# Performance work log

Hardware: AMD Instinct MI355X
Metric: run time of the kernel (lower is better)

## Reference

```python
import jax, jax.numpy as jnp
import numpy as np

EPS = 1e-12  # matches F.normalize default eps

def _l2norm(x):
    n = jnp.linalg.norm(x, axis=-1, keepdims=True)
    return x / jnp.maximum(n, EPS)

def setup_inputs() -> dict:
    key = jax.random.key(0)
    kq, kk, kv = jax.random.split(key, 3)
    B, N, D = 16384, 8192, 1024
    return {
        "query": jax.random.normal(kq, (B, D), dtype=jnp.float32),
        "keys": jax.random.normal(kk, (N, D), dtype=jnp.float32),
        "values": jax.random.normal(kv, (N, D), dtype=jnp.float32),
        "k": 4,
    }

def reference(query, keys, values, k):
    # cosine similarity: (B, N)
    qn = _l2norm(query)
    kn = _l2norm(keys)
    sim = jnp.einsum('bd,nd->bn', qn, kn)
    actual_k = min(k, sim.shape[1])
    topk_sim, topk_idx = jax.lax.top_k(sim, actual_k)     # (B, k)
    weights = jax.nn.softmax(topk_sim, axis=-1)            # (B, k)
    topk_vals = values[topk_idx]                           # (B, k, D)
    return jnp.einsum('bk,bkd->bd', weights, topk_vals)    # (B, D)
```

## Files before the change

kernel.cpp:

```cpp
#include <hip/hip_runtime.h>
#include <hip/hip_bf16.h>
#include <math.h>


#define D_DIM 1024
#define SLICES 8
#define BQ 128
#define BK 128
#define BD 64
#define TLIST 4
#define CAND_PER_Q (SLICES * TLIST)

typedef float f32x4 __attribute__((ext_vector_type(4)));
typedef short s16x8 __attribute__((ext_vector_type(8)));

typedef const __attribute__((address_space(1))) void* as1cv;
typedef __attribute__((address_space(3))) void* as3v;

__device__ __forceinline__ void gload_lds16(const void* g, void* l) {
    __builtin_amdgcn_global_load_lds((as1cv)g, (as3v)l, 16, 0, 0);
}

__device__ __forceinline__ unsigned short f2bf(float x) {
    unsigned int u;
    __builtin_memcpy(&u, &x, 4);
    unsigned int r = (u + 0x7fffu + ((u >> 16) & 1u)) >> 16;
    return (unsigned short)r;
}

__global__ __launch_bounds__(256) void nrm_kernel(
    const float* __restrict__ q, const float* __restrict__ kmat,
    unsigned short* __restrict__ qn, unsigned short* __restrict__ kn,
    float* __restrict__ inv_qn, float* __restrict__ inv_kn, int B, int N) {
    int wid = threadIdx.x >> 6, lane = threadIdx.x & 63;
    int row = blockIdx.x * 4 + wid;
    if (row >= B + N) return;
    const float* src;
    unsigned short* dst;
    float* invp;
    if (row < B) {
        src = q + (size_t)row * D_DIM; dst = qn + (size_t)row * D_DIM; invp = inv_qn + row;
    } else {
        int r = row - B;
        src = kmat + (size_t)r * D_DIM; dst = kn + (size_t)r * D_DIM; invp = inv_kn + r;
    }
    float4 v[4];
    float ss = 0.f;
#pragma unroll
    for (int c = 0; c < 4; ++c) {
        v[c] = *(const float4*)(src + c * 256 + lane * 4);
        ss += v[c].x * v[c].x + v[c].y * v[c].y + v[c].z * v[c].z + v[c].w * v[c].w;
    }
#pragma unroll
    for (int m = 1; m < 64; m <<= 1) ss += __shfl_xor(ss, m, 64);
    float s = 1.0f / fmaxf(sqrtf(ss), 1e-12f);
    if (lane == 0) *invp = s;
#pragma unroll
    for (int c = 0; c < 4; ++c) {
        ushort4 o;
        o.x = f2bf(v[c].x * s); o.y = f2bf(v[c].y * s);
        o.z = f2bf(v[c].z * s); o.w = f2bf(v[c].w * s);
        *(ushort4*)(dst + c * 256 + lane * 4) = o;
    }
}

__global__ __launch_bounds__(256, 4) void score_kernel(
    const unsigned short* __restrict__ qn, const unsigned short* __restrict__ kn,
    float* __restrict__ cand_s, int* __restrict__ cand_i, int B, int N) {
    __shared__ __attribute__((aligned(16))) unsigned char smem[33792];
    unsigned short* Kt = (unsigned short*)smem;
    unsigned short* Qt = (unsigned short*)(smem + 16384);
    float* ms = (float*)smem;
    int* mi = (int*)(smem + 16896);

    int bx = blockIdx.x;
    int qblk = bx >> 3, slice = bx & 7;
    int tid = threadIdx.x, wid = tid >> 6, lane = tid & 63;
    int wr = wid & 1, wc = wid >> 1;
    int slice_len = N / SLICES;
    int kbase0 = slice * slice_len;
    int qbase = qblk * BQ;
    int lg = lane >> 4;

    float ts[4][TLIST];
    int   ti[4][TLIST];
#pragma unroll
    for (int cg = 0; cg < 4; ++cg)
#pragma unroll
        for (int t = 0; t < TLIST; ++t) { ts[cg][t] = -1e30f; ti[cg][t] = 0; }

    for (int kt = 0; kt < slice_len / BK; ++kt) {
        int kb = kbase0 + kt * BK;
        f32x4 acc[4][4];
#pragma unroll
        for (int a = 0; a < 4; ++a)
#pragma unroll
            for (int b = 0; b < 4; ++b) acc[a][b] = (f32x4){0.f, 0.f, 0.f, 0.f};

        for (int dc = 0; dc < D_DIM / BD; ++dc) {
            int db = dc * BD;
#pragma unroll
            for (int i = 0; i < 4; ++i) {
                int te = (i * 4 + wid) * 64 + lane;
                int r = te >> 3, sl = te & 7;
                int c = (sl ^ (r & 7)) * 8;
                gload_lds16(kn + (size_t)(kb + r) * D_DIM + db + c, &Kt[(i * 4 + wid) * 512]);
            }
#pragma unroll
            for (int i = 0; i < 4; ++i) {
                int te = (i * 4 + wid) * 64 + lane;
                int r = te >> 3, sl = te & 7;
                int c = (sl ^ (r & 7)) * 8;
                gload_lds16(qn + (size_t)(qbase + r) * D_DIM + db + c, &Qt[(i * 4 + wid) * 512]);
            }
            __syncthreads();
#pragma unroll
            for (int ks = 0; ks < 2; ++ks) {
                int kslot = ks * 4 + lg;
                s16x8 afr[4], bfr[4];
#pragma unroll
                for (int rb = 0; rb < 4; ++rb) {
                    int row = wr * 64 + rb * 16 + (lane & 15);
                    afr[rb] = *(const s16x8*)&Kt[row * BD + ((kslot ^ (row & 7)) * 8)];
                }
#pragma unroll
                for (int cg = 0; cg < 4; ++cg) {
                    int row = wc * 64 + cg * 16 + (lane & 15);
                    bfr[cg] = *(const s16x8*)&Qt[row * BD + ((kslot ^ (row & 7)) * 8)];
                }
#pragma unroll
                for (int rb = 0; rb < 4; ++rb)
#pragma unroll
                    for (int cg = 0; cg < 4; ++cg)
                        acc[rb][cg] = __builtin_amdgcn_mfma_f32_16x16x32_bf16(
                            afr[rb], bfr[cg], acc[rb][cg], 0, 0, 0);
            }
            __syncthreads();
        }
#pragma unroll
        for (int rb = 0; rb < 4; ++rb) {
#pragma unroll
            for (int j = 0; j < 4; ++j) {
                int key = kb + wr * 64 + rb * 16 + (lg << 2) + j;
#pragma unroll
                for (int cg = 0; cg < 4; ++cg) {
                    float s = acc[rb][cg][j];
                    if (s > ts[cg][TLIST - 1]) {
                        int id = key;
#pragma unroll
                        for (int t = 0; t < TLIST; ++t) {
                            bool c = s > ts[cg][t];
                            float hi = c ? s : ts[cg][t];
                            float lo = c ? ts[cg][t] : s;
                            int ih = c ? id : ti[cg][t];
                            int il = c ? ti[cg][t] : id;
                            ts[cg][t] = hi; ti[cg][t] = ih; s = lo; id = il;
                        }
                    }
                }
            }
        }
    }

    __syncthreads();
#pragma unroll
    for (int cg = 0; cg < 4; ++cg) {
        int ql = wc * 64 + cg * 16 + (lane & 15);
        int slot = wr * 16 + lg * 4;
#pragma unroll
        for (int t = 0; t < TLIST; ++t) {
            ms[ql * 33 + slot + t] = ts[cg][t];
            mi[ql * 33 + slot + t] = ti[cg][t];
        }
    }
    __syncthreads();
    if (tid < BQ) {
        float bs[4] = {-1e30f, -1e30f, -1e30f, -1e30f};
        int bi4[4] = {0, 0, 0, 0};
#pragma unroll
        for (int s = 0; s < 32; ++s) {
            float v = ms[tid * 33 + s];
            int id = mi[tid * 33 + s];
            if (v > bs[3]) {
#pragma unroll
                for (int t = 0; t < 4; ++t) {
                    bool c = v > bs[t];
                    float hi = c ? v : bs[t];
                    float lo = c ? bs[t] : v;
                    int ih = c ? id : bi4[t];
                    int il = c ? bi4[t] : id;
                    bs[t] = hi; bi4[t] = ih; v = lo; id = il;
                }
            }
        }
        size_t base = (size_t)(qbase + tid) * CAND_PER_Q + slice * TLIST;
#pragma unroll
        for (int t = 0; t < 4; ++t) {
            cand_s[base + t] = bs[t];
            cand_i[base + t] = bi4[t];
        }
    }
}

__global__ __launch_bounds__(256) void final_kernel(
    const float* __restrict__ q, const float* __restrict__ kmat, const float* __restrict__ vmat,
    const float* __restrict__ inv_qn, const float* __restrict__ inv_kn,
    const float* __restrict__ cand_s, const int* __restrict__ cand_i,
    const int* __restrict__ kptr, float* __restrict__ out, int B, int N) {
    int wid = threadIdx.x >> 6, lane = threadIdx.x & 63;
    int qi = blockIdx.x * 4 + wid;
    int kk = *kptr;
    kk = kk < 1 ? 1 : (kk > 8 ? 8 : kk);

    size_t cb = (size_t)qi * CAND_PER_Q;
    float cs = lane < 32 ? cand_s[cb + lane] : -1e30f;
    int ci = lane < 32 ? cand_i[cb + lane] : 0x7fffffff;

    int rank = 0;
#pragma unroll
    for (int j = 0; j < 32; ++j) {
        float sj = __shfl(cs, j, 64);
        int ij = __shfl(ci, j, 64);
        rank += ((sj > cs) || (sj == cs && ij < ci)) ? 1 : 0;
    }
    int sel[8];
#pragma unroll
    for (int r = 0; r < 8; ++r) {
        unsigned long long m = __ballot(lane < 32 && rank == r);
        int ln = (int)__builtin_ctzll(m);
        sel[r] = __shfl(ci, ln, 64);
    }

    const float* qrow = q + (size_t)qi * D_DIM;
    float4 qv[4];
#pragma unroll
    for (int c = 0; c < 4; ++c) qv[c] = *(const float4*)(qrow + c * 256 + lane * 4);
    const float* kr[8];
#pragma unroll
    for (int r = 0; r < 8; ++r) kr[r] = kmat + (size_t)sel[r] * D_DIM;
    float p[8];
#pragma unroll
    for (int r = 0; r < 8; ++r) p[r] = 0.f;
#pragma unroll
    for (int e = 0; e < 4; ++e) {
#pragma unroll
        for (int r = 0; r < 8; ++r) {
            float4 kv = *(const float4*)(kr[r] + e * 256 + lane * 4);
            p[r] += qv[e].x * kv.x + qv[e].y * kv.y + qv[e].z * kv.z + qv[e].w * kv.w;
        }
    }
#pragma unroll
    for (int m = 1; m < 64; m <<= 1) {
#pragma unroll
        for (int r = 0; r < 8; ++r) p[r] += __shfl_xor(p[r], m, 64);
    }
    float invq = inv_qn[qi];
    float exsc[8];
#pragma unroll
    for (int r = 0; r < 8; ++r) exsc[r] = p[r] * invq * inv_kn[sel[r]];

    float wl[8]; int il[8]; bool used[8];
#pragma unroll
    for (int i = 0; i < 8; ++i) used[i] = false;
#pragma unroll
    for (int i = 0; i < 8; ++i) {
        int bj = 0; float bv = -1e30f; int bidx = 0x7fffffff;
#pragma unroll
        for (int j = 0; j < 8; ++j) {
            if (!used[j] && (exsc[j] > bv || (exsc[j] == bv && sel[j] < bidx))) {
                bv = exsc[j]; bidx = sel[j]; bj = j;
            }
        }
        used[bj] = true; wl[i] = bv; il[i] = bidx;
    }
    float m0 = wl[0], ssum = 0.f;
#pragma unroll
    for (int i = 0; i < 8; ++i) {
        wl[i] = (i < kk) ? __expf(wl[i] - m0) : 0.f;
        ssum += wl[i];
    }
    float rs = 1.0f / ssum;

    float4 o[4];
#pragma unroll
    for (int c = 0; c < 4; ++c) o[c] = (float4){0.f, 0.f, 0.f, 0.f};
#pragma unroll
    for (int i = 0; i < 8; ++i) {
        if (i < kk) {
            const float* vrow = vmat + (size_t)il[i] * D_DIM;
            float wi = wl[i] * rs;
#pragma unroll
            for (int c = 0; c < 4; ++c) {
                float4 vv = *(const float4*)(vrow + c * 256 + lane * 4);
                o[c].x += wi * vv.x; o[c].y += wi * vv.y;
                o[c].z += wi * vv.z; o[c].w += wi * vv.w;
            }
        }
    }
    float* orow = out + (size_t)qi * D_DIM;
#pragma unroll
    for (int c = 0; c < 4; ++c) *(float4*)(orow + c * 256 + lane * 4) = o[c];
}

extern "C" void kernel_launch(void* const* d_in, const int* in_sizes, int n_in,
                              void* d_out, int out_size, void* d_ws, size_t ws_size,
                              hipStream_t stream) {
    const float* q = (const float*)d_in[0];
    const float* kmat = (const float*)d_in[1];
    const float* vmat = (const float*)d_in[2];
    const int* kptr = (const int*)d_in[3];
    float* out = (float*)d_out;
    int B = in_sizes[0] / D_DIM;
    int N = in_sizes[1] / D_DIM;

    char* ws = (char*)d_ws;
    size_t off = 0;
    unsigned short* qn = (unsigned short*)(ws + off); off += (size_t)B * D_DIM * 2;
    unsigned short* kn = (unsigned short*)(ws + off); off += (size_t)N * D_DIM * 2;
    float* inv_qn = (float*)(ws + off); off += (size_t)B * 4;
    float* inv_kn = (float*)(ws + off); off += (size_t)N * 4;
    float* cand_s = (float*)(ws + off); off += (size_t)B * CAND_PER_Q * 4;
    int* cand_i = (int*)(ws + off); off += (size_t)B * CAND_PER_Q * 4;

    int rows = B + N;
    nrm_kernel<<<dim3((rows + 3) / 4), dim3(256), 0, stream>>>(q, kmat, qn, kn, inv_qn, inv_kn, B, N);
    score_kernel<<<dim3((B / BQ) * SLICES), dim3(256), 0, stream>>>(qn, kn, cand_s, cand_i, B, N);
    final_kernel<<<dim3(B / 4), dim3(256), 0, stream>>>(q, kmat, vmat, inv_qn, inv_kn,
                                                        cand_s, cand_i, kptr, out, B, N);
}
```

Measured before the change: 683.0 us.

## Enlarge score tiles to 256x256 with double-buffered LDS and wave-level top-k skip

New measurement: 651.1 us. 4.7% less time.

```diff
diff --git a/kernel.cpp b/kernel.cpp
--- a/kernel.cpp
+++ b/kernel.cpp
@@ -5,8 +5,8 @@
 
 #define D_DIM 1024
 #define SLICES 8
-#define BQ 128
-#define BK 128
+#define BQ 256
+#define BK 256
 #define BD 64
 #define TLIST 4
 #define CAND_PER_Q (SLICES * TLIST)
@@ -64,23 +64,21 @@
     }
 }
 
-__global__ __launch_bounds__(256, 4) void score_kernel(
+__global__ __launch_bounds__(512, 2) void score_kernel(
     const unsigned short* __restrict__ qn, const unsigned short* __restrict__ kn,
     float* __restrict__ cand_s, int* __restrict__ cand_i, int B, int N) {
-    __shared__ __attribute__((aligned(16))) unsigned char smem[33792];
-    unsigned short* Kt = (unsigned short*)smem;
-    unsigned short* Qt = (unsigned short*)(smem + 16384);
+    __shared__ __attribute__((aligned(16))) unsigned char smem[131072];
     float* ms = (float*)smem;
-    int* mi = (int*)(smem + 16896);
+    int* mi = (int*)(smem + 33792);
 
     int bx = blockIdx.x;
     int qblk = bx >> 3, slice = bx & 7;
     int tid = threadIdx.x, wid = tid >> 6, lane = tid & 63;
     int wr = wid & 1, wc = wid >> 1;
+    int lg = lane >> 4, l15 = lane & 15;
     int slice_len = N / SLICES;
     int kbase0 = slice * slice_len;
     int qbase = qblk * BQ;
-    int lg = lane >> 4;
 
     float ts[4][TLIST];
     int   ti[4][TLIST];
@@ -89,72 +87,90 @@
 #pragma unroll
         for (int t = 0; t < TLIST; ++t) { ts[cg][t] = -1e30f; ti[cg][t] = 0; }
 
+    auto STAGE = [&](int c, int kb, int db) {
+        unsigned short* KtD = (unsigned short*)(smem + c * 65536);
+        unsigned short* QtD = (unsigned short*)(smem + 32768 + c * 65536);
+#pragma unroll
+        for (int i = 0; i < 4; ++i) {
+            int te = i * 512 + tid;
+            int r = te >> 3, sl = te & 7;
+            int col = (sl ^ (r & 7)) * 8;
+            gload_lds16(kn + (size_t)(kb + r) * D_DIM + db + col, &KtD[i * 4096 + wid * 512]);
+        }
+#pragma unroll
+        for (int i = 0; i < 4; ++i) {
+            int te = i * 512 + tid;
+            int r = te >> 3, sl = te & 7;
+            int col = (sl ^ (r & 7)) * 8;
+            gload_lds16(qn + (size_t)(qbase + r) * D_DIM + db + col, &QtD[i * 4096 + wid * 512]);
+        }
+    };
+
     for (int kt = 0; kt < slice_len / BK; ++kt) {
         int kb = kbase0 + kt * BK;
-        f32x4 acc[4][4];
-#pragma unroll
-        for (int a = 0; a < 4; ++a)
+        f32x4 acc[8][4];
+#pragma unroll
+        for (int a = 0; a < 8; ++a)
 #pragma unroll
             for (int b = 0; b < 4; ++b) acc[a][b] = (f32x4){0.f, 0.f, 0.f, 0.f};
 
+        STAGE(0, kb, 0);
+        __syncthreads();
+        int cur = 0;
         for (int dc = 0; dc < D_DIM / BD; ++dc) {
-            int db = dc * BD;
-#pragma unroll
-            for (int i = 0; i < 4; ++i) {
-                int te = (i * 4 + wid) * 64 + lane;
-                int r = te >> 3, sl = te & 7;
-                int c = (sl ^ (r & 7)) * 8;
-                gload_lds16(kn + (size_t)(kb + r) * D_DIM + db + c, &Kt[(i * 4 + wid) * 512]);
-            }
-#pragma unroll
-            for (int i = 0; i < 4; ++i) {
-                int te = (i * 4 + wid) * 64 + lane;
-                int r = te >> 3, sl = te & 7;
-                int c = (sl ^ (r & 7)) * 8;
-                gload_lds16(qn + (size_t)(qbase + r) * D_DIM + db + c, &Qt[(i * 4 + wid) * 512]);
-            }
-            __syncthreads();
+            if (dc + 1 < D_DIM / BD) STAGE(cur ^ 1, kb, (dc + 1) * BD);
+            const unsigned short* KtC = (const unsigned short*)(smem + cur * 65536);
+            const unsigned short* QtC = (const unsigned short*)(smem + 32768 + cur * 65536);
 #pragma unroll
             for (int ks = 0; ks < 2; ++ks) {
                 int kslot = ks * 4 + lg;
-                s16x8 afr[4], bfr[4];
-#pragma unroll
-                for (int rb = 0; rb < 4; ++rb) {
-                    int row = wr * 64 + rb * 16 + (lane & 15);
-                    afr[rb] = *(const s16x8*)&Kt[row * BD + ((kslot ^ (row & 7)) * 8)];
+                s16x8 afr[8], bfr[4];
+#pragma unroll
+                for (int rb = 0; rb < 8; ++rb) {
+                    int row = wr * 128 + rb * 16 + l15;
+                    afr[rb] = *(const s16x8*)&KtC[row * BD + ((kslot ^ (row & 7)) * 8)];
                 }
 #pragma unroll
                 for (int cg = 0; cg < 4; ++cg) {
-                    int row = wc * 64 + cg * 16 + (lane & 15);
-                    bfr[cg] = *(const s16x8*)&Qt[row * BD + ((kslot ^ (row & 7)) * 8)];
+                    int row = wc * 64 + cg * 16 + l15;
+                    bfr[cg] = *(const s16x8*)&QtC[row * BD + ((kslot ^ (row & 7)) * 8)];
                 }
-#pragma unroll
-                for (int rb = 0; rb < 4; ++rb)
+                __builtin_amdgcn_s_setprio(1);
+#pragma unroll
+                for (int rb = 0; rb < 8; ++rb)
 #pragma unroll
                     for (int cg = 0; cg < 4; ++cg)
                         acc[rb][cg] = __builtin_amdgcn_mfma_f32_16x16x32_bf16(
                             afr[rb], bfr[cg], acc[rb][cg], 0, 0, 0);
+                __builtin_amdgcn_s_setprio(0);
             }
             __syncthreads();
-        }
-#pragma unroll
-        for (int rb = 0; rb < 4; ++rb) {
-#pragma unroll
-            for (int j = 0; j < 4; ++j) {
-                int key = kb + wr * 64 + rb * 16 + (lg << 2) + j;
-#pragma unroll
-                for (int cg = 0; cg < 4; ++cg) {
-                    float s = acc[rb][cg][j];
-                    if (s > ts[cg][TLIST - 1]) {
-                        int id = key;
-#pragma unroll
-                        for (int t = 0; t < TLIST; ++t) {
-                            bool c = s > ts[cg][t];
-                            float hi = c ? s : ts[cg][t];
-                            float lo = c ? ts[cg][t] : s;
-                            int ih = c ? id : ti[cg][t];
-                            int il = c ? ti[cg][t] : id;
-                            ts[cg][t] = hi; ti[cg][t] = ih; s = lo; id = il;
+            cur ^= 1;
+        }
+#pragma unroll
+        for (int cg = 0; cg < 4; ++cg) {
+            float mx = acc[0][cg][0];
+#pragma unroll
+            for (int rb = 0; rb < 8; ++rb)
+#pragma unroll
+                for (int j = 0; j < 4; ++j) mx = fmaxf(mx, acc[rb][cg][j]);
+            if (__any(mx > ts[cg][TLIST - 1])) {
+#pragma unroll
+                for (int rb = 0; rb < 8; ++rb) {
+#pragma unroll
+                    for (int j = 0; j < 4; ++j) {
+                        float s = acc[rb][cg][j];
+                        if (s > ts[cg][TLIST - 1]) {
+                            int id = kb + wr * 128 + rb * 16 + (lg << 2) + j;
+#pragma unroll
+                            for (int t = 0; t < TLIST; ++t) {
+                                bool c = s > ts[cg][t];
+                                float hi = c ? s : ts[cg][t];
+                                float lo = c ? ts[cg][t] : s;
+                                int ih = c ? id : ti[cg][t];
+                                int il = c ? ti[cg][t] : id;
+                                ts[cg][t] = hi; ti[cg][t] = ih; s = lo; id = il;
+                            }
                         }
                     }
                 }
@@ -165,7 +181,7 @@
     __syncthreads();
 #pragma unroll
     for (int cg = 0; cg < 4; ++cg) {
-        int ql = wc * 64 + cg * 16 + (lane & 15);
+        int ql = wc * 64 + cg * 16 + l15;
         int slot = wr * 16 + lg * 4;
 #pragma unroll
         for (int t = 0; t < TLIST; ++t) {
@@ -324,7 +340,7 @@
 
     int rows = B + N;
     nrm_kernel<<<dim3((rows + 3) / 4), dim3(256), 0, stream>>>(q, kmat, qn, kn, inv_qn, inv_kn, B, N);
-    score_kernel<<<dim3((B / BQ) * SLICES), dim3(256), 0, stream>>>(qn, kn, cand_s, cand_i, B, N);
+    score_kernel<<<dim3((B / BQ) * SLICES), dim3(512), 0, stream>>>(qn, kn, cand_s, cand_i, B, N);
     final_kernel<<<dim3(B / 4), dim3(256), 0, stream>>>(q, kmat, vmat, inv_qn, inv_kn,
                                                         cand_s, cand_i, kptr, out, B, N);
 }
```
